# Performance work log

Hardware: AMD Instinct MI355X
Metric: run time of the kernel (lower is better)

The kernel has to match this reference:

```python
import jax, jax.numpy as jnp
import numpy as np

B, T, D, H = 4, 2048, 1024, 16
HD = D // H


def setup_inputs() -> dict:
    key = jax.random.key(0)
    ks = jax.random.split(key, 10)
    s = 1.0 / np.sqrt(D)
    # xavier_uniform bound for wbias [T,T]: sqrt(6/(T+T))
    wb_bound = float(np.sqrt(6.0 / (T + T)))
    return {
        "x": jax.random.normal(ks[0], (B, T, D), dtype=jnp.float32),
        "Wq": jax.random.normal(ks[1], (D, D), dtype=jnp.float32) * s,
        "bq": jnp.zeros((D,), dtype=jnp.float32),
        "Wk": jax.random.normal(ks[2], (D, D), dtype=jnp.float32) * s,
        "bk": jnp.zeros((D,), dtype=jnp.float32),
        "Wv": jax.random.normal(ks[3], (D, D), dtype=jnp.float32) * s,
        "bv": jnp.zeros((D,), dtype=jnp.float32),
        "Wo": jax.random.normal(ks[4], (D, D), dtype=jnp.float32) * s,
        "bo": jnp.zeros((D,), dtype=jnp.float32),
        "wbias": jax.random.uniform(ks[5], (T, T), dtype=jnp.float32,
                                    minval=-wb_bound, maxval=wb_bound),
    }


def reference(x, Wq, bq, Wk, bk, Wv, bv, Wo, bo, wbias):
    Bc, Tc, Dc = x.shape
    # projections, split heads: [B, H, T, HD]
    def proj(W, b):
        y = x @ W + b
        return y.reshape(Bc, Tc, H, HD).transpose(0, 2, 1, 3)

    Q = proj(Wq, bq)
    K = proj(Wk, bk)
    V = proj(Wv, bv)

    Q_sig = jax.nn.sigmoid(Q)
    eK = jnp.exp(K)                      # [B,H,T,HD]
    ew = jnp.exp(wbias[:Tc, :Tc])        # [T,T]

    num = jnp.einsum('ts,bhsd->bhtd', ew, eK * V)
    den = jnp.einsum('ts,bhsd->bhtd', ew, eK)
    out = Q_sig * (num / den)            # [B,H,T,HD]

    out = out.transpose(0, 2, 1, 3).reshape(Bc, Tc, Dc)
    return out @ Wo + bo
```

## Files before the change

### kernel.cpp

```cpp
#include <hip/hip_runtime.h>
#include <hip/hip_bf16.h>


#define AS1(p) ((const __attribute__((address_space(1))) void*)(p))
#define AS3(p) ((__attribute__((address_space(3))) void*)(p))

typedef _Float16 half8 __attribute__((ext_vector_type(8)));
typedef _Float16 half4v __attribute__((ext_vector_type(4)));
typedef float floatx16 __attribute__((ext_vector_type(16)));

__device__ __forceinline__ long frag_off(int r, int k) {
  return (long)(((((r >> 5) * 4 + (k >> 4)) * 2 + ((k >> 3) & 1)) * 32 + (r & 31)) * 8 + (k & 7));
}

__global__ void prep_tiles(const float* __restrict__ x, const float* __restrict__ wb,
                           _Float16* __restrict__ x_h, _Float16* __restrict__ ew_h) {
  const int bid = blockIdx.x;
  const int tid = threadIdx.x;
  const bool isx = bid < 1024;
  const float* src;
  _Float16* dst;
  int tm, tk, ld, trel;
  if (isx) {
    trel = bid; tm = bid >> 4; tk = bid & 15; src = x; dst = x_h; ld = 1024;
  } else {
    trel = bid - 1024; tm = trel >> 5; tk = trel & 31; src = wb; dst = ew_h; ld = 2048;
  }
  const long tbase = (long)trel * 8192;
#pragma unroll
  for (int p = 0; p < 4; ++p) {
    const int s = p * 256 + tid;
    const int r = ((s >> 8) << 5) + (s & 31);
    const int k = ((s >> 6) & 3) * 16 + ((s >> 5) & 1) * 8;
    const float* sp = src + (long)(tm * 128 + r) * ld + tk * 64 + k;
    const float4 v0 = *(const float4*)sp;
    const float4 v1 = *(const float4*)(sp + 4);
    half8 h;
    if (isx) {
      h[0] = (_Float16)v0.x; h[1] = (_Float16)v0.y; h[2] = (_Float16)v0.z; h[3] = (_Float16)v0.w;
      h[4] = (_Float16)v1.x; h[5] = (_Float16)v1.y; h[6] = (_Float16)v1.z; h[7] = (_Float16)v1.w;
    } else {
      h[0] = (_Float16)__expf(v0.x); h[1] = (_Float16)__expf(v0.y);
      h[2] = (_Float16)__expf(v0.z); h[3] = (_Float16)__expf(v0.w);
      h[4] = (_Float16)__expf(v1.x); h[5] = (_Float16)__expf(v1.y);
      h[6] = (_Float16)__expf(v1.z); h[7] = (_Float16)__expf(v1.w);
    }
    *(half8*)(dst + tbase + (long)s * 8) = h;
  }
}

__global__ void transpose_cast_w(const float* __restrict__ w0, const float* __restrict__ w1,
                                 const float* __restrict__ w2, const float* __restrict__ w3,
                                 _Float16* __restrict__ dqkv, _Float16* __restrict__ dwo) {
  const int z = blockIdx.z;
  const float* src = z == 0 ? w0 : z == 1 ? w1 : z == 2 ? w2 : w3;
  __shared__ float tile[32][33];
  const int r0 = blockIdx.x * 32, c0 = blockIdx.y * 32;
  const int tr = threadIdx.x >> 5, tc = threadIdx.x & 31;
#pragma unroll
  for (int p = 0; p < 4; ++p) {
    int rr = tr + p * 8;
    tile[rr][tc] = src[(size_t)(r0 + rr) * 1024 + c0 + tc];
  }
  __syncthreads();
#pragma unroll
  for (int p = 0; p < 4; ++p) {
    const int c = c0 + tr + p * 8;
    const int kk = r0 + tc;
    int jr;
    _Float16* dst;
    if (z == 0) { jr = c; dst = dqkv; }
    else if (z == 3) { jr = c; dst = dwo; }
    else { jr = 1024 + ((c >> 5) << 6) + ((z == 2) ? 32 : 0) + (c & 31); dst = dqkv; }
    const long addr = ((long)(jr >> 7) * 16 + (kk >> 6)) * 8192 + frag_off(jr & 127, kk & 63);
    dst[addr] = (_Float16)tile[tc][tr + p * 8];
  }
}

template <int MODE>
__global__ __launch_bounds__(256) void gemm_bt(
    const _Float16* __restrict__ A, const _Float16* __restrict__ Bt, void* __restrict__ Cv,
    int Ktiles, long batchB, const float* __restrict__ bias0, const float* __restrict__ bias1,
    const float* __restrict__ bias2, const _Float16* __restrict__ Qsig,
    _Float16* __restrict__ Zt) {
  __shared__ __align__(16) _Float16 sA[8192];
  __shared__ __align__(16) _Float16 sB[8192];
  const int tid = threadIdx.x;
  const int wave = tid >> 6, lane = tid & 63;
  const int l32 = lane & 31, khalf = lane >> 5;
  const int m0 = blockIdx.x * 128, n0 = blockIdx.y * 128;
  const int wm = (wave >> 1) * 64, wn = (wave & 1) * 64;

  const _Float16* Atile = A + (long)blockIdx.x * Ktiles * 8192;
  const _Float16* Btile = Bt + (long)blockIdx.z * batchB + (long)blockIdx.y * Ktiles * 8192;

  floatx16 acc[2][2] = {};

  for (int tk = 0; tk < Ktiles; ++tk) {
    const _Float16* As = Atile + tk * 8192 + wave * 512 + lane * 8;
    const _Float16* Bs = Btile + tk * 8192 + wave * 512 + lane * 8;
#pragma unroll
    for (int c = 0; c < 4; ++c) {
      __builtin_amdgcn_global_load_lds(AS1(As + c * 2048), AS3(sA + c * 2048 + wave * 512), 16, 0, 0);
      __builtin_amdgcn_global_load_lds(AS1(Bs + c * 2048), AS3(sB + c * 2048 + wave * 512), 16, 0, 0);
    }
    __syncthreads();
#pragma unroll
    for (int ks = 0; ks < 4; ++ks) {
      half8 af[2], bf[2];
#pragma unroll
      for (int i = 0; i < 2; ++i) {
        af[i] = *(const half8*)(sA + (((wm >> 5) + i) * 4 + ks) * 512 + lane * 8);
        bf[i] = *(const half8*)(sB + (((wn >> 5) + i) * 4 + ks) * 512 + lane * 8);
      }
#pragma unroll
      for (int mt = 0; mt < 2; ++mt)
#pragma unroll
        for (int nt = 0; nt < 2; ++nt)
          acc[mt][nt] =
              __builtin_amdgcn_mfma_f32_32x32x16_f16(af[mt], bf[nt], acc[mt][nt], 0, 0, 0);
    }
    __syncthreads();
  }

  if (MODE == 0) {
    if (n0 < 1024) {
      _Float16* Qs = (_Float16*)Cv;
#pragma unroll
      for (int mt = 0; mt < 2; ++mt)
#pragma unroll
        for (int nt = 0; nt < 2; ++nt) {
          const int col = n0 + wn + nt * 32 + l32;
          const float bb = bias0[col];
#pragma unroll
          for (int reg = 0; reg < 16; ++reg) {
            const int row = m0 + wm + mt * 32 + 4 * khalf + 8 * (reg >> 2) + (reg & 3);
            const float v = acc[mt][nt][reg] + bb;
            Qs[(long)row * 1024 + col] = (_Float16)(1.0f / (1.0f + __expf(-v)));
          }
        }
    } else {
      const int g = (n0 - 1024 + wn) >> 6;
      const int ch = g * 32 + l32;
      const float bkc = bias1[ch], bvc = bias2[ch];
      const int jn = g * 64 + l32;
      const long tnbase = (long)(jn >> 7) * 32 * 8192;
#pragma unroll
      for (int mt = 0; mt < 2; ++mt) {
#pragma unroll
        for (int q = 0; q < 4; ++q) {
          half4v numv, denv;
#pragma unroll
          for (int rr = 0; rr < 4; ++rr) {
            const float ek = __expf(acc[mt][0][q * 4 + rr] + bkc);
            const float vv = acc[mt][1][q * 4 + rr] + bvc;
            denv[rr] = (_Float16)ek;
            numv[rr] = (_Float16)(ek * vv);
          }
          const int row = m0 + wm + mt * 32 + 4 * khalf + 8 * q;
          const int b = row >> 11, s = row & 2047;
          const long off = (long)b * 4194304 + tnbase + (long)(s >> 6) * 8192 +
                           frag_off(jn & 127, s & 63);
          *(half4v*)(Zt + off) = numv;
          *(half4v*)(Zt + off + 2048) = denv;
        }
      }
    }
    return;
  }

  if (MODE == 3) {
    const _Float16* Q = Qsig + (long)blockIdx.z * 2097152;
    const int ch = ((n0 + wn) >> 6) * 32 + l32;
    _Float16* OH = (_Float16*)Cv;
#pragma unroll
    for (int mt = 0; mt < 2; ++mt)
#pragma unroll
      for (int reg = 0; reg < 16; ++reg) {
        const int r = m0 + wm + mt * 32 + 4 * khalf + 8 * (reg >> 2) + (reg & 3);
        const float num = acc[mt][0][reg], den = acc[mt][1][reg];
        const float qs = (float)Q[(long)r * 1024 + ch];
        const int R = blockIdx.z * 2048 + r;
        const long off = ((long)(R >> 7) * 16 + (ch >> 6)) * 8192 + frag_off(R & 127, ch & 63);
        OH[off] = (_Float16)(qs * num / den);
      }
    return;
  }

#pragma unroll
  for (int mt = 0; mt < 2; ++mt)
#pragma unroll
    for (int nt = 0; nt < 2; ++nt) {
      const int col = n0 + wn + nt * 32 + l32;
      const float bb = bias0[col];
#pragma unroll
      for (int reg = 0; reg < 16; ++reg) {
        const int row = m0 + wm + mt * 32 + 4 * khalf + 8 * (reg >> 2) + (reg & 3);
        ((float*)Cv)[(long)row * 1024 + col] = acc[mt][nt][reg] + bb;
      }
    }
}

extern "C" void kernel_launch(void* const* d_in, const int* in_sizes, int n_in, void* d_out,
                              int out_size, void* d_ws, size_t ws_size, hipStream_t stream) {
  const float* x = (const float*)d_in[0];
  const float* Wq = (const float*)d_in[1];
  const float* bq = (const float*)d_in[2];
  const float* Wk = (const float*)d_in[3];
  const float* bk = (const float*)d_in[4];
  const float* Wv = (const float*)d_in[5];
  const float* bv = (const float*)d_in[6];
  const float* Wo = (const float*)d_in[7];
  const float* bo = (const float*)d_in[8];
  const float* wb = (const float*)d_in[9];

  char* ws = (char*)d_ws;
  _Float16* x_h = (_Float16*)(ws + 0);
  _Float16* WqkvT = (_Float16*)(ws + 16777216);
  _Float16* WoT = (_Float16*)(ws + 23068672);
  _Float16* ew_h = (_Float16*)(ws + 25165824);
  _Float16* Qsig = (_Float16*)(ws + 33554432);
  _Float16* Zt = (_Float16*)(ws + 50331648);
  _Float16* OutHead = (_Float16*)(ws + 83886080);

  prep_tiles<<<1536, 256, 0, stream>>>(x, wb, x_h, ew_h);
  transpose_cast_w<<<dim3(32, 32, 4), 256, 0, stream>>>(Wq, Wk, Wv, Wo, WqkvT, WoT);

  gemm_bt<0><<<dim3(64, 24, 1), 256, 0, stream>>>(x_h, WqkvT, Qsig, 16, 0, bq, bk, bv, nullptr,
                                                  Zt);

  gemm_bt<3><<<dim3(16, 16, 4), 256, 0, stream>>>(ew_h, Zt, OutHead, 32, (long)4194304, nullptr,
                                                  nullptr, nullptr, Qsig, nullptr);

  gemm_bt<2><<<dim3(64, 8, 1), 256, 0, stream>>>(OutHead, WoT, d_out, 16, 0, bo, nullptr,
                                                 nullptr, nullptr, nullptr);
}
```

Before: 301.7 us.

## Merge prep kernels, remap GEMM blocks across XCDs, tile Qsig layout for vector stores

Merges the input-tile conversion and the weight transpose-cast into one launch. The weight transpose now goes through a larger LDS tile with vectorized float4 reads and half8 writes instead of scalar 16-bit stores. GEMM block indices are remapped so consecutive blocks are spread across the 8 chiplets (XCDs), aiming for better L2 locality. Qsig is stored in a fragment-tiled layout so the QKV epilogue can write, and the attention epilogue read, half4 vectors instead of scattered scalars. The block remap assumes the total block count divides by 8, and it changes the layout of an intermediate buffer that two kernels must agree on.

```diff
diff --git a/kernel.cpp b/kernel.cpp
--- a/kernel.cpp
+++ b/kernel.cpp
@@ -13,67 +13,102 @@
   return (long)(((((r >> 5) * 4 + (k >> 4)) * 2 + ((k >> 3) & 1)) * 32 + (r & 31)) * 8 + (k & 7));
 }
 
-__global__ void prep_tiles(const float* __restrict__ x, const float* __restrict__ wb,
-                           _Float16* __restrict__ x_h, _Float16* __restrict__ ew_h) {
+
+__global__ __launch_bounds__(256) void prep_all(
+    const float* __restrict__ x, const float* __restrict__ wb, const float* __restrict__ Wq,
+    const float* __restrict__ Wk, const float* __restrict__ Wv, const float* __restrict__ Wo,
+    _Float16* __restrict__ x_h, _Float16* __restrict__ ew_h, _Float16* __restrict__ WqkvT,
+    _Float16* __restrict__ WoT) {
+  __shared__ _Float16 lds[64 * 132];
   const int bid = blockIdx.x;
   const int tid = threadIdx.x;
-  const bool isx = bid < 1024;
-  const float* src;
+
+  if (bid < 1536) {
+    const bool isx = bid < 1024;
+    const float* src;
+    _Float16* dst;
+    int tm, tk, ld, trel;
+    if (isx) {
+      trel = bid; tm = bid >> 4; tk = bid & 15; src = x; dst = x_h; ld = 1024;
+    } else {
+      trel = bid - 1024; tm = trel >> 5; tk = trel & 31; src = wb; dst = ew_h; ld = 2048;
+    }
+    const long tbase = (long)trel * 8192;
+#pragma unroll
+    for (int p = 0; p < 4; ++p) {
+      const int s = p * 256 + tid;
+      const int r = ((s >> 8) << 5) + (s & 31);
+      const int k = ((s >> 6) & 3) * 16 + ((s >> 5) & 1) * 8;
+      const float* sp = src + (long)(tm * 128 + r) * ld + tk * 64 + k;
+      const float4 v0 = *(const float4*)sp;
+      const float4 v1 = *(const float4*)(sp + 4);
+      half8 h;
+      if (isx) {
+        h[0] = (_Float16)v0.x; h[1] = (_Float16)v0.y; h[2] = (_Float16)v0.z; h[3] = (_Float16)v0.w;
+        h[4] = (_Float16)v1.x; h[5] = (_Float16)v1.y; h[6] = (_Float16)v1.z; h[7] = (_Float16)v1.w;
+      } else {
+        h[0] = (_Float16)__expf(v0.x); h[1] = (_Float16)__expf(v0.y);
+        h[2] = (_Float16)__expf(v0.z); h[3] = (_Float16)__expf(v0.w);
+        h[4] = (_Float16)__expf(v1.x); h[5] = (_Float16)__expf(v1.y);
+        h[6] = (_Float16)__expf(v1.z); h[7] = (_Float16)__expf(v1.w);
+      }
+      *(half8*)(dst + tbase + (long)s * 8) = h;
+    }
+    return;
+  }
+
+  const int b2 = bid - 1536;
+  const float* src0;
+  const float* src1 = nullptr;
   _Float16* dst;
-  int tm, tk, ld, trel;
-  if (isx) {
-    trel = bid; tm = bid >> 4; tk = bid & 15; src = x; dst = x_h; ld = 1024;
+  int tn, tk, cb = 0;
+  if (b2 < 128) {
+    tn = b2 >> 4; tk = b2 & 15; src0 = Wq; dst = WqkvT;
+  } else if (b2 < 384) {
+    const int t = b2 - 128;
+    tn = 8 + (t >> 4); tk = t & 15; cb = (tn - 8) * 64; src0 = Wk; src1 = Wv; dst = WqkvT;
   } else {
-    trel = bid - 1024; tm = trel >> 5; tk = trel & 31; src = wb; dst = ew_h; ld = 2048;
-  }
-  const long tbase = (long)trel * 8192;
+    const int t = b2 - 384;
+    tn = t >> 4; tk = t & 15; src0 = Wo; dst = WoT;
+  }
+  if (!src1) {
+#pragma unroll
+    for (int p = 0; p < 8; ++p) {
+      const int kl = p * 8 + (tid >> 5);
+      const int cl = (tid & 31) * 4;
+      const float4 v = *(const float4*)(src0 + (long)(tk * 64 + kl) * 1024 + tn * 128 + cl);
+      half4v h;
+      h[0] = (_Float16)v.x; h[1] = (_Float16)v.y; h[2] = (_Float16)v.z; h[3] = (_Float16)v.w;
+      *(half4v*)(lds + kl * 132 + cl) = h;
+    }
+  } else {
+#pragma unroll
+    for (int m = 0; m < 2; ++m) {
+      const float* s = m ? src1 : src0;
+      const int rb = m ? 32 : 0;
+#pragma unroll
+      for (int p = 0; p < 4; ++p) {
+        const int kl = p * 16 + (tid >> 4);
+        const int cl = (tid & 15) * 4;
+        const int rl = (cl >> 5) * 64 + rb + (cl & 31);
+        const float4 v = *(const float4*)(s + (long)(tk * 64 + kl) * 1024 + cb + cl);
+        half4v h;
+        h[0] = (_Float16)v.x; h[1] = (_Float16)v.y; h[2] = (_Float16)v.z; h[3] = (_Float16)v.w;
+        *(half4v*)(lds + kl * 132 + rl) = h;
+      }
+    }
+  }
+  __syncthreads();
+  const long tbase = (long)(tn * 16 + tk) * 8192;
 #pragma unroll
   for (int p = 0; p < 4; ++p) {
     const int s = p * 256 + tid;
     const int r = ((s >> 8) << 5) + (s & 31);
-    const int k = ((s >> 6) & 3) * 16 + ((s >> 5) & 1) * 8;
-    const float* sp = src + (long)(tm * 128 + r) * ld + tk * 64 + k;
-    const float4 v0 = *(const float4*)sp;
-    const float4 v1 = *(const float4*)(sp + 4);
+    const int kl = ((s >> 6) & 3) * 16 + ((s >> 5) & 1) * 8;
     half8 h;
-    if (isx) {
-      h[0] = (_Float16)v0.x; h[1] = (_Float16)v0.y; h[2] = (_Float16)v0.z; h[3] = (_Float16)v0.w;
-      h[4] = (_Float16)v1.x; h[5] = (_Float16)v1.y; h[6] = (_Float16)v1.z; h[7] = (_Float16)v1.w;
-    } else {
-      h[0] = (_Float16)__expf(v0.x); h[1] = (_Float16)__expf(v0.y);
-      h[2] = (_Float16)__expf(v0.z); h[3] = (_Float16)__expf(v0.w);
-      h[4] = (_Float16)__expf(v1.x); h[5] = (_Float16)__expf(v1.y);
-      h[6] = (_Float16)__expf(v1.z); h[7] = (_Float16)__expf(v1.w);
-    }
+#pragma unroll
+    for (int j = 0; j < 8; ++j) h[j] = lds[(kl + j) * 132 + r];
     *(half8*)(dst + tbase + (long)s * 8) = h;
-  }
-}
-
-__global__ void transpose_cast_w(const float* __restrict__ w0, const float* __restrict__ w1,
-                                 const float* __restrict__ w2, const float* __restrict__ w3,
-                                 _Float16* __restrict__ dqkv, _Float16* __restrict__ dwo) {
-  const int z = blockIdx.z;
-  const float* src = z == 0 ? w0 : z == 1 ? w1 : z == 2 ? w2 : w3;
-  __shared__ float tile[32][33];
-  const int r0 = blockIdx.x * 32, c0 = blockIdx.y * 32;
-  const int tr = threadIdx.x >> 5, tc = threadIdx.x & 31;
-#pragma unroll
-  for (int p = 0; p < 4; ++p) {
-    int rr = tr + p * 8;
-    tile[rr][tc] = src[(size_t)(r0 + rr) * 1024 + c0 + tc];
-  }
-  __syncthreads();
-#pragma unroll
-  for (int p = 0; p < 4; ++p) {
-    const int c = c0 + tr + p * 8;
-    const int kk = r0 + tc;
-    int jr;
-    _Float16* dst;
-    if (z == 0) { jr = c; dst = dqkv; }
-    else if (z == 3) { jr = c; dst = dwo; }
-    else { jr = 1024 + ((c >> 5) << 6) + ((z == 2) ? 32 : 0) + (c & 31); dst = dqkv; }
-    const long addr = ((long)(jr >> 7) * 16 + (kk >> 6)) * 8192 + frag_off(jr & 127, kk & 63);
-    dst[addr] = (_Float16)tile[tc][tr + p * 8];
   }
 }
 
@@ -88,11 +123,20 @@
   const int tid = threadIdx.x;
   const int wave = tid >> 6, lane = tid & 63;
   const int l32 = lane & 31, khalf = lane >> 5;
-  const int m0 = blockIdx.x * 128, n0 = blockIdx.y * 128;
+
+  const int gx = gridDim.x, gy = gridDim.y;
+  const int tot = gx * gy * gridDim.z;
+  const int f = blockIdx.x + gx * (blockIdx.y + gy * blockIdx.z);
+  const int nid = (f & 7) * (tot >> 3) + (f >> 3);
+  const int bxs = nid % gx;
+  const int bys = (nid / gx) % gy;
+  const int bzs = nid / (gx * gy);
+
+  const int m0 = bxs * 128, n0 = bys * 128;
   const int wm = (wave >> 1) * 64, wn = (wave & 1) * 64;
 
-  const _Float16* Atile = A + (long)blockIdx.x * Ktiles * 8192;
-  const _Float16* Btile = Bt + (long)blockIdx.z * batchB + (long)blockIdx.y * Ktiles * 8192;
+  const _Float16* Atile = A + (long)bxs * Ktiles * 8192;
+  const _Float16* Btile = Bt + (long)bzs * batchB + (long)bys * Ktiles * 8192;
 
   floatx16 acc[2][2] = {};
 
@@ -127,18 +171,25 @@
     if (n0 < 1024) {
       _Float16* Qs = (_Float16*)Cv;
 #pragma unroll
-      for (int mt = 0; mt < 2; ++mt)
+      for (int mt = 0; mt < 2; ++mt) {
+        const long ttile = (m0 + wm + mt * 32) >> 5;
 #pragma unroll
         for (int nt = 0; nt < 2; ++nt) {
           const int col = n0 + wn + nt * 32 + l32;
           const float bb = bias0[col];
-#pragma unroll
-          for (int reg = 0; reg < 16; ++reg) {
-            const int row = m0 + wm + mt * 32 + 4 * khalf + 8 * (reg >> 2) + (reg & 3);
-            const float v = acc[mt][nt][reg] + bb;
-            Qs[(long)row * 1024 + col] = (_Float16)(1.0f / (1.0f + __expf(-v)));
+          const long base = (ttile * 32 + (((n0 + wn) >> 5) + nt)) * 1024;
+#pragma unroll
+          for (int q = 0; q < 4; ++q) {
+            half4v o;
+#pragma unroll
+            for (int rr = 0; rr < 4; ++rr) {
+              const float v = acc[mt][nt][q * 4 + rr] + bb;
+              o[rr] = (_Float16)(1.0f / (1.0f + __expf(-v)));
+            }
+            *(half4v*)(Qs + base + q * 256 + lane * 4) = o;
           }
         }
+      }
     } else {
       const int g = (n0 - 1024 + wn) >> 6;
       const int ch = g * 32 + l32;
@@ -170,20 +221,26 @@
   }
 
   if (MODE == 3) {
-    const _Float16* Q = Qsig + (long)blockIdx.z * 2097152;
     const int ch = ((n0 + wn) >> 6) * 32 + l32;
     _Float16* OH = (_Float16*)Cv;
 #pragma unroll
-    for (int mt = 0; mt < 2; ++mt)
-#pragma unroll
-      for (int reg = 0; reg < 16; ++reg) {
-        const int r = m0 + wm + mt * 32 + 4 * khalf + 8 * (reg >> 2) + (reg & 3);
-        const float num = acc[mt][0][reg], den = acc[mt][1][reg];
-        const float qs = (float)Q[(long)r * 1024 + ch];
-        const int R = blockIdx.z * 2048 + r;
-        const long off = ((long)(R >> 7) * 16 + (ch >> 6)) * 8192 + frag_off(R & 127, ch & 63);
-        OH[off] = (_Float16)(qs * num / den);
-      }
+    for (int mt = 0; mt < 2; ++mt) {
+      const long ttile = (long)(bzs * 2048 + m0 + wm + mt * 32) >> 5;
+      const long qbase = (ttile * 32 + ((n0 + wn) >> 6)) * 1024;
+#pragma unroll
+      for (int q = 0; q < 4; ++q) {
+        const half4v qv = *(const half4v*)(Qsig + qbase + q * 256 + lane * 4);
+#pragma unroll
+        for (int rr = 0; rr < 4; ++rr) {
+          const int reg = q * 4 + rr;
+          const float num = acc[mt][0][reg], den = acc[mt][1][reg];
+          const int r = m0 + wm + mt * 32 + 4 * khalf + 8 * q + rr;
+          const int R = bzs * 2048 + r;
+          const long off = ((long)(R >> 7) * 16 + (ch >> 6)) * 8192 + frag_off(R & 127, ch & 63);
+          OH[off] = (_Float16)((float)qv[rr] * num / den);
+        }
+      }
+    }
     return;
   }
 
@@ -223,8 +280,7 @@
   _Float16* Zt = (_Float16*)(ws + 50331648);
   _Float16* OutHead = (_Float16*)(ws + 83886080);
 
-  prep_tiles<<<1536, 256, 0, stream>>>(x, wb, x_h, ew_h);
-  transpose_cast_w<<<dim3(32, 32, 4), 256, 0, stream>>>(Wq, Wk, Wv, Wo, WqkvT, WoT);
+  prep_all<<<2048, 256, 0, stream>>>(x, wb, Wq, Wk, Wv, Wo, x_h, ew_h, WqkvT, WoT);
 
   gemm_bt<0><<<dim3(64, 24, 1), 256, 0, stream>>>(x_h, WqkvT, Qsig, 16, 0, bq, bk, bv, nullptr,
                                                   Zt);
```

Measured after the change: 293.9 us. 2.6% less time.
